# Optimization experiments

Measured on AMD Instinct MI355X. Metric: run time of the kernel, lower is better.

Reference implementation:

```python
import jax, jax.numpy as jnp
import numpy as np

N = 100000   # nodes
E = 1250000  # edges
G = 64       # graphs in batch
F_IN, H, NT, GT = 29, 64, 6, 4
L = 4        # num GCN layers


def setup_inputs() -> dict:
    key = jax.random.key(0)
    ks = jax.random.split(key, 14)
    s_in = 1.0 / np.sqrt(F_IN)
    s_h = 1.0 / np.sqrt(H)
    return {
        "x": jax.random.normal(ks[0], (N, F_IN), dtype=jnp.float32),
        "edge_index": jax.random.randint(ks[1], (2, E), 0, N, dtype=jnp.int64),
        "batch": jnp.sort(jax.random.randint(ks[2], (N,), 0, G, dtype=jnp.int64)),
        "encW": jax.random.uniform(ks[3], (F_IN, H), jnp.float32, -s_in, s_in),
        "encb": jax.random.uniform(ks[4], (H,), jnp.float32, -s_in, s_in),
        "convW": jax.random.uniform(ks[5], (L, H, H), jnp.float32, -s_h, s_h),
        "convb": jax.random.uniform(ks[6], (L, H), jnp.float32, -s_h, s_h),
        "nodeW": jax.random.uniform(ks[7], (H, NT), jnp.float32, -s_h, s_h),
        "nodeb": jax.random.uniform(ks[8], (NT,), jnp.float32, -s_h, s_h),
        "g1W": jax.random.uniform(ks[9], (H, H), jnp.float32, -s_h, s_h),
        "g1b": jax.random.uniform(ks[10], (H,), jnp.float32, -s_h, s_h),
        "g2W": jax.random.uniform(ks[11], (H, GT), jnp.float32, -s_h, s_h),
        "g2b": jax.random.uniform(ks[12], (GT,), jnp.float32, -s_h, s_h),
    }


def reference(x, edge_index, batch, encW, encb, convW, convb, nodeW, nodeb, g1W, g1b, g2W, g2b):
    # GCNConv with self-loops and symmetric normalization (PyG defaults)
    loop = jnp.arange(N, dtype=edge_index.dtype)
    row = jnp.concatenate([edge_index[0], loop])  # senders
    col = jnp.concatenate([edge_index[1], loop])  # receivers
    deg = jax.ops.segment_sum(jnp.ones_like(col, dtype=x.dtype), col, num_segments=N)
    dis = jnp.where(deg > 0, deg ** -0.5, 0.0)
    norm = (dis[row] * dis[col])[:, None]  # [E+N, 1]

    h = jax.nn.relu(x @ encW + encb)
    for i in range(L):
        hw = h @ convW[i]  # transform then propagate
        agg = jax.ops.segment_sum(hw[row] * norm, col, num_segments=N)
        h = jax.nn.relu(agg + convb[i])

    pred_node = h @ nodeW + nodeb

    counts = jax.ops.segment_sum(jnp.ones((N,), x.dtype), batch, num_segments=G)
    gemb = jax.ops.segment_sum(h, batch, num_segments=G) / jnp.maximum(counts, 1.0)[:, None]
    pred_global = jax.nn.relu(gemb @ g1W + g1b) @ g2W + g2b
    return (pred_node, pred_global)
```

## Files before the change

kernel.cpp:

```cpp
#include <hip/hip_runtime.h>
#include <hip/hip_fp16.h>

#define N_NODES 100000
#define N_EDGES 1250000
#define N_GRAPHS 64
#define F_INN 29
#define HD 64
#define NT 6
#define GT 4
#define NLAYERS 4
#define RECS_CAP 3000000
#define NBLK 1563
#define NBUK 782
#define HGRID 256
#define GB_BLOCKS 391
#define ENC_BLOCKS 6250
#define NH_BLOCKS 3125

typedef __attribute__((ext_vector_type(8))) _Float16 f16x8;
typedef __attribute__((ext_vector_type(4))) float f32x4;

__global__ void hist1_misc(const int* __restrict__ col, int* __restrict__ ghistT, int E,
                           const float* __restrict__ convW, uint4* __restrict__ wfrag,
                           __half* __restrict__ ht1, __half* __restrict__ ht2,
                           const int* __restrict__ batch, int* __restrict__ start) {
    __shared__ int lh[NBUK];
    int tid = threadIdx.x, b = blockIdx.x;
    if (b < HGRID) {
        for (int i = tid; i < NBUK; i += 256) lh[i] = 0;
        __syncthreads();
        for (int e = b * 256 + tid; e < E; e += HGRID * 256) atomicAdd(&lh[col[e] >> 7], 1);
        __syncthreads();
        for (int i = tid; i < NBUK; i += 256) ghistT[i * 256 + b] = lh[i];
    } else if (b < HGRID + 4) {
        int layer = b - HGRID;
        const float* W = convW + (size_t)layer * HD * HD;
        uint4* out = wfrag + (size_t)layer * 512;
        for (int s = tid; s < 512; s += 256) {
            int jt = s >> 7, ks = (s >> 6) & 1, l = s & 63;
            int j = jt * 16 + (l & 15);
            int k0 = ks * 32 + (l >> 4) * 8;
            __align__(16) __half hh[8];
            #pragma unroll
            for (int i = 0; i < 8; ++i) hh[i] = __float2half_rn(W[(size_t)(k0 + i) * HD + j]);
            out[s] = *reinterpret_cast<const uint4*>(hh);
        }
    } else if (b == HGRID + 4) {
        if (tid < HD) ht1[(size_t)N_NODES * HD + tid] = __float2half_rn(0.f);
        else if (tid < 2 * HD) ht2[(size_t)N_NODES * HD + (tid - HD)] = __float2half_rn(0.f);
    } else {
        int i = (b - HGRID - 5) * 256 + tid;
        if (i < N_NODES) {
            int bb = batch[i];
            if (i == 0) {
                for (int g = 0; g <= bb; ++g) start[g] = 0;
            } else {
                int pb = batch[i - 1];
                if (pb != bb) for (int g = pb + 1; g <= bb; ++g) start[g] = i;
            }
            if (i == N_NODES - 1) {
                for (int g = bb + 1; g <= N_GRAPHS; ++g) start[g] = N_NODES;
            }
        }
    }
}

__global__ void hist_colscan(int* __restrict__ ghistT, int* __restrict__ tot) {
    __shared__ int wsum[4];
    int k = blockIdx.x, tid = threadIdx.x;
    int v = ghistT[k * 256 + tid];
    int incl = v;
    int lane = tid & 63;
    #pragma unroll
    for (int off = 1; off < 64; off <<= 1) {
        int t = __shfl_up(incl, (unsigned)off, 64);
        if (lane >= off) incl += t;
    }
    if (lane == 63) wsum[tid >> 6] = incl;
    __syncthreads();
    int woff = 0;
    for (int w = 0; w < (tid >> 6); ++w) woff += wsum[w];
    ghistT[k * 256 + tid] = woff + incl - v;
    if (tid == 255) tot[k] = woff + incl;
}

__global__ void scan1(const int* __restrict__ in, int* __restrict__ out,
                      int* __restrict__ bsums, int n) {
    __shared__ int wsum[4];
    int tid = threadIdx.x;
    int base = blockIdx.x * 1024 + tid * 4;
    int v0 = (base + 0 < n) ? in[base + 0] : 0;
    int v1 = (base + 1 < n) ? in[base + 1] : 0;
    int v2 = (base + 2 < n) ? in[base + 2] : 0;
    int v3 = (base + 3 < n) ? in[base + 3] : 0;
    int tsum = v0 + v1 + v2 + v3;
    int incl = tsum;
    int lane = tid & 63;
    #pragma unroll
    for (int off = 1; off < 64; off <<= 1) {
        int t = __shfl_up(incl, (unsigned)off, 64);
        if (lane >= off) incl += t;
    }
    if (lane == 63) wsum[tid >> 6] = incl;
    __syncthreads();
    int woff = 0;
    for (int w = 0; w < (tid >> 6); ++w) woff += wsum[w];
    int run = woff + incl - tsum;
    if (base + 0 < n) out[base + 0] = run; run += v0;
    if (base + 1 < n) out[base + 1] = run; run += v1;
    if (base + 2 < n) out[base + 2] = run; run += v2;
    if (base + 3 < n) out[base + 3] = run;
    if (tid == 255) bsums[blockIdx.x] = woff + incl;
}

__global__ void scatter_buckets(const int* __restrict__ row, const int* __restrict__ col,
                                const int* __restrict__ ghistT, const int* __restrict__ boff,
                                unsigned* __restrict__ bke, int E) {
    __shared__ int cur[NBUK];
    int tid = threadIdx.x, b = blockIdx.x;
    for (int i = tid; i < NBUK; i += 256) cur[i] = ghistT[i * 256 + b] + boff[i];
    __syncthreads();
    for (int e = b * 256 + tid; e < E; e += HGRID * 256) {
        int c = col[e];
        int pos = atomicAdd(&cur[c >> 7], 1);
        bke[pos] = (unsigned)row[e] | ((unsigned)(c & 127) << 25);
    }
}

__global__ void bucket_count(const unsigned* __restrict__ bke, const int* __restrict__ boff,
                             int* __restrict__ cnt16, float* __restrict__ dis,
                             int* __restrict__ btot, int E) {
    __shared__ int lc[128];
    __shared__ int red[2];
    int k = blockIdx.x, tid = threadIdx.x;
    if (tid < 128) lc[tid] = 0;
    __syncthreads();
    int s = boff[k];
    int t = (k == NBUK - 1) ? E : boff[k + 1];
    for (int i = s + tid; i < t; i += 256) atomicAdd(&lc[bke[i] >> 25], 1);
    __syncthreads();
    int c16 = 0;
    if (tid < 128) {
        int node = k * 128 + tid;
        if (node < N_NODES) {
            int c = lc[tid];
            c16 = (c + 15) & ~15;
            cnt16[node] = c16;
            dis[node] = rsqrtf((float)(c + 1));
        }
        int sum = c16;
        #pragma unroll
        for (int off = 1; off < 64; off <<= 1) sum += __shfl_xor(sum, off, 64);
        if ((tid & 63) == 0) red[tid >> 6] = sum;
    }
    __syncthreads();
    if (tid == 0) btot[k] = red[0] + red[1];
}

__global__ void fill_enc(const unsigned* __restrict__ bke, const int* __restrict__ boff,
                         const int* __restrict__ bbase, const int* __restrict__ cnt16,
                         int* __restrict__ offs, int* __restrict__ srcs, int E,
                         const float* __restrict__ x, const float* __restrict__ encW,
                         const float* __restrict__ encb, const float* __restrict__ dis,
                         __half* __restrict__ ht) {
    int tid = threadIdx.x;
    int b = blockIdx.x;
    if (b < NBUK) {
        __shared__ int offsL[128];
        __shared__ int cur[128];
        __shared__ int wtot[2];
        int k = b;
        int v = 0, incl = 0;
        if (tid < 128) {
            int node = k * 128 + tid;
            v = (node < N_NODES) ? cnt16[node] : 0;
            incl = v;
            int lane = tid & 63;
            #pragma unroll
            for (int off = 1; off < 64; off <<= 1) {
                int t = __shfl_up(incl, (unsigned)off, 64);
                if (lane >= off) incl += t;
            }
            if (lane == 63) wtot[tid >> 6] = incl;
        }
        __syncthreads();
        if (tid < 128) {
            int w0 = (tid >= 64) ? wtot[0] : 0;
            int node = k * 128 + tid;
            int o = bbase[k] + w0 + incl - v;
            offsL[tid] = o;
            cur[tid] = 0;
            if (node < N_NODES) offs[node] = o;
        }
        __syncthreads();
        int s = boff[k];
        int t = (k == NBUK - 1) ? E : boff[k + 1];
        for (int i = s + tid; i < t; i += 256) {
            unsigned u = bke[i];
            int l = u >> 25;
            int r = atomicAdd(&cur[l], 1);
            srcs[offsL[l] + r] = (int)(u & 0x01FFFFFFu);
        }
        __syncthreads();
        if (tid < 128) {
            int node = k * 128 + tid;
            if (node < N_NODES) {
                int c = cur[tid];
                int c16 = (c + 15) & ~15;
                int base = offsL[tid];
                for (int p = base + c; p < base + c16; ++p) srcs[p] = N_NODES;
            }
        }
    } else {
        __shared__ float Ws[F_INN * HD];
        __shared__ float bs[HD];
        __shared__ float xs[16 * F_INN];
        for (int i = tid; i < F_INN * HD; i += 256) Ws[i] = encW[i];
        if (tid < HD) bs[tid] = encb[tid];
        int n0 = (b - NBUK) * 16;
        for (int i = tid; i < 16 * F_INN; i += 256) {
            int nn = n0 + i / F_INN;
            xs[i] = (nn < N_NODES) ? x[(size_t)nn * F_INN + (i % F_INN)] : 0.f;
        }
        __syncthreads();
        #pragma unroll
        for (int it = 0; it < 4; ++it) {
            int l = it * 4 + (tid >> 6);
            int j = tid & 63;
            int nn = n0 + l;
            if (nn < N_NODES) {
                float a = bs[j];
                #pragma unroll
                for (int k = 0; k < F_INN; ++k) a = fmaf(xs[l * F_INN + k], Ws[k * HD + j], a);
                ht[(size_t)nn * HD + j] = __float2half_rn(dis[nn] * fmaxf(a, 0.f));
            }
        }
    }
}


__device__ __forceinline__ float4 cvtrow(uint2 u) {
    float2 a = __half22float2(*reinterpret_cast<const __half2*>(&u.x));
    float2 b = __half22float2(*reinterpret_cast<const __half2*>(&u.y));
    return make_float4(a.x, a.y, b.x, b.y);
}

#define ROW16(src) (*reinterpret_cast<const uint2*>(&ht[(size_t)(src) * HD + fh]))
#define H2(u) (*reinterpret_cast<const __half2*>(&(u)))
#define ACC4T(r0, r1, r2, r3) { \
    __half2 ax = __hadd2(__hadd2(H2(r0.x), H2(r1.x)), __hadd2(H2(r2.x), H2(r3.x))); \
    __half2 ay = __hadd2(__hadd2(H2(r0.y), H2(r1.y)), __hadd2(H2(r2.y), H2(r3.y))); \
    float2 fx = __half22float2(ax); \
    float2 fy = __half22float2(ay); \
    acc.x += fx.x; acc.y += fx.y; acc.z += fy.x; acc.w += fy.y; }

__global__ void layer_kernel(const __half* __restrict__ ht,
                             const int* __restrict__ offs, const int* __restrict__ cnt16,
                             const int4* __restrict__ srcs4,
                             const float* __restrict__ dis,
                             const uint4* __restrict__ wfragL, const float* __restrict__ bias,
                             __half* __restrict__ hout, int scaleOut) {
    __shared__ uint4 WfS[512];
    __shared__ __half aggS[64 * 72];
    __shared__ int offsS[64];
    __shared__ int cntS[64];
    __shared__ float disS[64];
    int tid = threadIdx.x;
    int b = blockIdx.x;
    WfS[tid] = wfragL[tid];
    WfS[tid + 256] = wfragL[tid + 256];
    if (tid < 64) {
        int d = b * 64 + tid;
        if (d < N_NODES) {
            offsS[tid] = offs[d];
            cntS[tid] = cnt16[d];
            disS[tid] = dis[d];
        } else {
            offsS[tid] = offs[N_NODES - 1] + cnt16[N_NODES - 1];
            cntS[tid] = 0;
            disS[tid] = 0.f;
        }
    }
    __syncthreads();

    int wave = tid >> 6;
    int lane = tid & 63;
    int q = lane >> 4;
    int fh = (lane & 15) * 4;

    int l0 = wave * 16 + q * 4;
    {
        int nbase = b * 64 + l0;
        *reinterpret_cast<uint2*>(&aggS[(l0 + 0) * 72 + fh]) = ROW16(min(nbase + 0, N_NODES));
        *reinterpret_cast<uint2*>(&aggS[(l0 + 1) * 72 + fh]) = ROW16(min(nbase + 1, N_NODES));
        *reinterpret_cast<uint2*>(&aggS[(l0 + 2) * 72 + fh]) = ROW16(min(nbase + 2, N_NODES));
        *reinterpret_cast<uint2*>(&aggS[(l0 + 3) * 72 + fh]) = ROW16(min(nbase + 3, N_NODES));
    }
    int s = offsS[l0];
    int e = offsS[l0 + 3] + cntS[l0 + 3];
    int dcur = l0;
    int nb = offsS[l0] + cntS[l0];
    float4 acc = {0.f, 0.f, 0.f, 0.f};

    auto flush = [&](int d) {
        uint2 sv = *reinterpret_cast<uint2*>(&aggS[d * 72 + fh]);
        float4 sf = cvtrow(sv);
        acc.x += sf.x; acc.y += sf.y; acc.z += sf.z; acc.w += sf.w;
        __half2 h0 = __floats2half2_rn(acc.x, acc.y);
        __half2 h1 = __floats2half2_rn(acc.z, acc.w);
        uint2 w;
        w.x = *(unsigned*)&h0;
        w.y = *(unsigned*)&h1;
        *reinterpret_cast<uint2*>(&aggS[d * 72 + fh]) = w;
        acc = make_float4(0.f, 0.f, 0.f, 0.f);
    };

    for (int p = s; p < e; p += 16) {
        while (p >= nb) {
            flush(dcur);
            ++dcur;
            nb = offsS[dcur] + cntS[dcur];
        }
        int base = p >> 2;
        int4 e0 = srcs4[base + 0];
        int4 e1 = srcs4[base + 1];
        int4 e2 = srcs4[base + 2];
        int4 e3 = srcs4[base + 3];
        uint2 r0 = ROW16(e0.x), r1 = ROW16(e0.y), r2 = ROW16(e0.z), r3 = ROW16(e0.w);
        uint2 r4 = ROW16(e1.x), r5 = ROW16(e1.y), r6 = ROW16(e1.z), r7 = ROW16(e1.w);
        uint2 r8 = ROW16(e2.x), r9 = ROW16(e2.y), r10 = ROW16(e2.z), r11 = ROW16(e2.w);
        uint2 r12 = ROW16(e3.x), r13 = ROW16(e3.y), r14 = ROW16(e3.z), r15 = ROW16(e3.w);
        ACC4T(r0, r1, r2, r3);
        ACC4T(r4, r5, r6, r7);
        ACC4T(r8, r9, r10, r11);
        ACC4T(r12, r13, r14, r15);
    }
    while (dcur <= l0 + 3) {
        flush(dcur);
        ++dcur;
    }
    __syncthreads();

    f32x4 c0 = {0.f, 0.f, 0.f, 0.f}, c1 = c0, c2 = c0, c3 = c0;
    #pragma unroll
    for (int ks = 0; ks < 2; ++ks) {
        f16x8 bf = *reinterpret_cast<const f16x8*>(&WfS[(wave * 2 + ks) * 64 + lane]);
        f16x8 a0 = *reinterpret_cast<const f16x8*>(&aggS[(0 * 16 + (lane & 15)) * 72 + ks * 32 + (lane >> 4) * 8]);
        c0 = __builtin_amdgcn_mfma_f32_16x16x32_f16(a0, bf, c0, 0, 0, 0);
        f16x8 a1 = *reinterpret_cast<const f16x8*>(&aggS[(1 * 16 + (lane & 15)) * 72 + ks * 32 + (lane >> 4) * 8]);
        c1 = __builtin_amdgcn_mfma_f32_16x16x32_f16(a1, bf, c1, 0, 0, 0);
        f16x8 a2 = *reinterpret_cast<const f16x8*>(&aggS[(2 * 16 + (lane & 15)) * 72 + ks * 32 + (lane >> 4) * 8]);
        c2 = __builtin_amdgcn_mfma_f32_16x16x32_f16(a2, bf, c2, 0, 0, 0);
        f16x8 a3 = *reinterpret_cast<const f16x8*>(&aggS[(3 * 16 + (lane & 15)) * 72 + ks * 32 + (lane >> 4) * 8]);
        c3 = __builtin_amdgcn_mfma_f32_16x16x32_f16(a3, bf, c3, 0, 0, 0);
    }
    int j = wave * 16 + (lane & 15);
    float bj = bias[j];
    #pragma unroll
    for (int nt = 0; nt < 4; ++nt) {
        f32x4 c = (nt == 0) ? c0 : (nt == 1) ? c1 : (nt == 2) ? c2 : c3;
        #pragma unroll
        for (int i = 0; i < 4; ++i) {
            int rl = nt * 16 + (lane >> 4) * 4 + i;
            int node = b * 64 + rl;
            if (node < N_NODES) {
                float dn = disS[rl];
                float o = fmaxf(fmaf(dn, c[i], bj), 0.f);
                if (scaleOut) o *= dn;
                hout[(size_t)node * HD + j] = __float2half_rn(o);
            }
        }
    }
}

__global__ void heads_kernel(const __half* __restrict__ h, const float* __restrict__ W,
                             const float* __restrict__ bb, float* __restrict__ out,
                             const int* __restrict__ start, float* __restrict__ gpart) {
    int tid = threadIdx.x;
    int b = blockIdx.x;
    if (b < NH_BLOCKS) {
        __shared__ float Ws[HD * NT];
        __shared__ float bs[NT];
        __shared__ float hs[32 * 65];
        for (int i = tid; i < HD * NT; i += 256) Ws[i] = W[i];
        if (tid < NT) bs[tid] = bb[tid];
        int n0 = b * 32;
        const unsigned* hrow = reinterpret_cast<const unsigned*>(&h[(size_t)n0 * HD]);
        for (int i = tid; i < 32 * HD / 2; i += 256) {
            unsigned u = hrow[i];
            float2 f = __half22float2(*reinterpret_cast<const __half2*>(&u));
            int el = i * 2;
            int row = el >> 6, colc = el & 63;
            hs[row * 65 + colc] = f.x;
            hs[row * 65 + colc + 1] = f.y;
        }
        __syncthreads();
        int l = tid >> 3, t = tid & 7;
        int nn = n0 + l;
        if (nn < N_NODES && t < NT) {
            float a = bs[t];
            #pragma unroll
            for (int k = 0; k < HD; ++k) a = fmaf(hs[l * 65 + k], Ws[k * NT + t], a);
            out[(size_t)nn * NT + t] = a;
        }
    } else {
        __shared__ float red[4][HD];
        int pb = b - NH_BLOCKS;
        int g = pb >> 2, q = pb & 3;
        int s0 = start[g], e0 = start[g + 1];
        int len = e0 - s0;
        int qs = s0 + (len * q) / 4;
        int qe = s0 + (len * (q + 1)) / 4;
        int wave = tid >> 6, lane = tid & 63;
        float acc = 0.f;
        for (int r = qs + wave; r < qe; r += 4) acc += __half2float(h[(size_t)r * HD + lane]);
        red[wave][lane] = acc;
        __syncthreads();
        if (wave == 0)
            gpart[(size_t)pb * HD + lane] =
                red[0][lane] + red[1][lane] + red[2][lane] + red[3][lane];
    }
}

__global__ void global_head(const float* __restrict__ gpart, const int* __restrict__ start,
                            const float* __restrict__ g1W, const float* __restrict__ g1b,
                            const float* __restrict__ g2W, const float* __restrict__ g2b,
                            float* __restrict__ out) {
    __shared__ float rS[HD];
    int g = blockIdx.x;
    int j = threadIdx.x;
    int cnt = start[g + 1] - start[g];
    float inv = 1.f / fmaxf((float)cnt, 1.f);
    rS[j] = (gpart[(size_t)(4 * g + 0) * HD + j] + gpart[(size_t)(4 * g + 1) * HD + j] +
             gpart[(size_t)(4 * g + 2) * HD + j] + gpart[(size_t)(4 * g + 3) * HD + j]) * inv;
    __syncthreads();
    float a = g1b[j];
    #pragma unroll
    for (int k = 0; k < HD; ++k) a = fmaf(rS[k], g1W[k * HD + j], a);
    a = fmaxf(a, 0.f);
    float o0 = a * g2W[j * GT + 0];
    float o1 = a * g2W[j * GT + 1];
    float o2 = a * g2W[j * GT + 2];
    float o3 = a * g2W[j * GT + 3];
    #pragma unroll
    for (int off = 1; off < 64; off <<= 1) {
        o0 += __shfl_xor(o0, off, 64);
        o1 += __shfl_xor(o1, off, 64);
        o2 += __shfl_xor(o2, off, 64);
        o3 += __shfl_xor(o3, off, 64);
    }
    if (j == 0) {
        out[g * GT + 0] = o0 + g2b[0];
        out[g * GT + 1] = o1 + g2b[1];
        out[g * GT + 2] = o2 + g2b[2];
        out[g * GT + 3] = o3 + g2b[3];
    }
}


extern "C" void kernel_launch(void* const* d_in, const int* in_sizes, int n_in,
                              void* d_out, int out_size, void* d_ws, size_t ws_size,
                              hipStream_t stream) {
    const float* x    = (const float*)d_in[0];
    const int*   ei   = (const int*)d_in[1];
    const int*   batch= (const int*)d_in[2];
    const float* encW = (const float*)d_in[3];
    const float* encb = (const float*)d_in[4];
    const float* convW= (const float*)d_in[5];
    const float* convb= (const float*)d_in[6];
    const float* nodeW= (const float*)d_in[7];
    const float* nodeb= (const float*)d_in[8];
    const float* g1W  = (const float*)d_in[9];
    const float* g1b  = (const float*)d_in[10];
    const float* g2W  = (const float*)d_in[11];
    const float* g2b  = (const float*)d_in[12];
    float* out = (float*)d_out;

    const int N = N_NODES, E = N_EDGES;

    char* ws = (char*)d_ws;
    size_t off = 0;
    auto alloc = [&](size_t bytes) -> void* {
        void* p = ws + off;
        off += (bytes + 255) & ~(size_t)255;
        return p;
    };
    int*    ghistT = (int*)alloc((size_t)NBUK * 256 * 4);
    int*    tot    = (int*)alloc((size_t)NBUK * 4);
    int*    boff   = (int*)alloc((size_t)NBUK * 4);
    int*    btot   = (int*)alloc((size_t)NBUK * 4);
    int*    bbase  = (int*)alloc((size_t)NBUK * 4);
    unsigned* bke  = (unsigned*)alloc((size_t)E * 4);
    int*    offs   = (int*)alloc((size_t)N * 4);
    int*    cnt16  = (int*)alloc((size_t)N * 4);
    float*  dis    = (float*)alloc((size_t)N * 4);
    int*    bsums  = (int*)alloc(256 * 4);
    int*    start  = (int*)alloc((size_t)(N_GRAPHS + 1) * 4);
    float*  gpart  = (float*)alloc((size_t)N_GRAPHS * 4 * HD * 4);
    uint4*  wfrag  = (uint4*)alloc((size_t)NLAYERS * 512 * 16);
    int*    srcs   = (int*)alloc((size_t)RECS_CAP * 4);
    __half* ht1    = (__half*)alloc((size_t)(N + 1) * HD * 2);
    __half* ht2    = (__half*)alloc((size_t)(N + 1) * HD * 2);

    hist1_misc<<<HGRID + 5 + GB_BLOCKS, 256, 0, stream>>>(ei + E, ghistT, E, convW, wfrag,
                                                          ht1, ht2, batch, start);
    hist_colscan<<<NBUK, 256, 0, stream>>>(ghistT, tot);
    scan1<<<1, 256, 0, stream>>>(tot, boff, bsums, NBUK);
    scatter_buckets<<<HGRID, 256, 0, stream>>>(ei, ei + E, ghistT, boff, bke, E);
    bucket_count<<<NBUK, 256, 0, stream>>>(bke, boff, cnt16, dis, btot, E);
    scan1<<<1, 256, 0, stream>>>(btot, bbase, bsums, NBUK);
    fill_enc<<<NBUK + ENC_BLOCKS, 256, 0, stream>>>(bke, boff, bbase, cnt16, offs, srcs, E,
                                                    x, encW, encb, dis, ht1);

    __half* hin = ht1;
    __half* hot = ht2;
    for (int i = 0; i < NLAYERS; ++i) {
        layer_kernel<<<NBLK, 256, 0, stream>>>(hin, offs, cnt16, (const int4*)srcs, dis,
                                               wfrag + (size_t)i * 512,
                                               convb + (size_t)i * HD,
                                               hot, (i < NLAYERS - 1) ? 1 : 0);
        __half* t = hin; hin = hot; hot = t;
    }

    heads_kernel<<<NH_BLOCKS + N_GRAPHS * 4, 256, 0, stream>>>(hin, nodeW, nodeb, out,
                                                               start, gpart);
    global_head<<<N_GRAPHS, 64, 0, stream>>>(gpart, start, g1W, g1b, g2W, g2b, out + (size_t)N * NT);
}
```

Baseline: 233.4 us.

## Partition each node's edge list by source chunk for cache locality in gather

Edges of each destination node are split into four segments by source-node range, with each segment padded to a multiple of 4 instead of 16. The layer kernel then gathers one source chunk at a time across all nodes in a block, so the set of feature rows touched at once fits better in cache. Padding waste drops, but the gather loop now issues fewer loads per iteration, there are more segment boundaries, and the block keeps fp32 partial sums in shared memory. Weight fragments are read from global memory instead of being staged in shared memory, and launch bounds are added to raise occupancy.

After: 248.3 us. +6.4%, slower.

```diff
diff --git a/kernel.cpp b/kernel.cpp
--- a/kernel.cpp
+++ b/kernel.cpp
@@ -2,6 +2,7 @@
 #include <hip/hip_fp16.h>
 
 #define N_NODES 100000
+#define N_CAP 100096
 #define N_EDGES 1250000
 #define N_GRAPHS 64
 #define F_INN 29
@@ -9,6 +10,8 @@
 #define NT 6
 #define GT 4
 #define NLAYERS 4
+#define NC 4
+#define CHUNK_SZ 25000
 #define RECS_CAP 3000000
 #define NBLK 1563
 #define NBUK 782
@@ -128,69 +131,89 @@
 }
 
 __global__ void bucket_count(const unsigned* __restrict__ bke, const int* __restrict__ boff,
-                             int* __restrict__ cnt16, float* __restrict__ dis,
+                             int* __restrict__ cnt4c, float* __restrict__ dis,
                              int* __restrict__ btot, int E) {
-    __shared__ int lc[128];
-    __shared__ int red[2];
+    __shared__ int lc[128 * NC];
+    __shared__ int red[4];
     int k = blockIdx.x, tid = threadIdx.x;
-    if (tid < 128) lc[tid] = 0;
+    for (int i = tid; i < 128 * NC; i += 256) lc[i] = 0;
     __syncthreads();
     int s = boff[k];
     int t = (k == NBUK - 1) ? E : boff[k + 1];
-    for (int i = s + tid; i < t; i += 256) atomicAdd(&lc[bke[i] >> 25], 1);
-    __syncthreads();
-    int c16 = 0;
+    for (int i = s + tid; i < t; i += 256) {
+        unsigned u = bke[i];
+        int l = u >> 25;
+        unsigned src = u & 0x01FFFFFFu;
+        atomicAdd(&lc[l * NC + (int)(src / CHUNK_SZ)], 1);
+    }
+    __syncthreads();
+    int padsum = 0;
+    for (int i = tid; i < 128 * NC; i += 256) {
+        int p4 = (lc[i] + 3) & ~3;
+        int node = k * 128 + (i >> 2);
+        cnt4c[(size_t)node * NC + (i & 3)] = p4;
+        padsum += p4;
+    }
     if (tid < 128) {
         int node = k * 128 + tid;
         if (node < N_NODES) {
-            int c = lc[tid];
-            c16 = (c + 15) & ~15;
-            cnt16[node] = c16;
-            dis[node] = rsqrtf((float)(c + 1));
-        }
-        int sum = c16;
-        #pragma unroll
-        for (int off = 1; off < 64; off <<= 1) sum += __shfl_xor(sum, off, 64);
-        if ((tid & 63) == 0) red[tid >> 6] = sum;
-    }
-    __syncthreads();
-    if (tid == 0) btot[k] = red[0] + red[1];
+            int deg = lc[tid * NC] + lc[tid * NC + 1] + lc[tid * NC + 2] + lc[tid * NC + 3];
+            dis[node] = rsqrtf((float)(deg + 1));
+        }
+    }
+    int lane = tid & 63;
+    #pragma unroll
+    for (int off = 1; off < 64; off <<= 1) padsum += __shfl_xor(padsum, off, 64);
+    if (lane == 0) red[tid >> 6] = padsum;
+    __syncthreads();
+    if (tid == 0) btot[k] = red[0] + red[1] + red[2] + red[3];
 }
 
 __global__ void fill_enc(const unsigned* __restrict__ bke, const int* __restrict__ boff,
-                         const int* __restrict__ bbase, const int* __restrict__ cnt16,
-                         int* __restrict__ offs, int* __restrict__ srcs, int E,
+                         const int* __restrict__ bbase, const int* __restrict__ cnt4c,
+                         int* __restrict__ segoff, int* __restrict__ srcs, int E,
                          const float* __restrict__ x, const float* __restrict__ encW,
                          const float* __restrict__ encb, const float* __restrict__ dis,
                          __half* __restrict__ ht) {
+    __shared__ int segL[512];
+    __shared__ int curO[512];
+    __shared__ int wsum[4];
+    __shared__ float Ws[F_INN * HD];
+    __shared__ float bs[HD];
+    __shared__ float xs[16 * F_INN];
     int tid = threadIdx.x;
     int b = blockIdx.x;
     if (b < NBUK) {
-        __shared__ int offsL[128];
-        __shared__ int cur[128];
-        __shared__ int wtot[2];
         int k = b;
-        int v = 0, incl = 0;
-        if (tid < 128) {
-            int node = k * 128 + tid;
-            v = (node < N_NODES) ? cnt16[node] : 0;
-            incl = v;
-            int lane = tid & 63;
-            #pragma unroll
-            for (int off = 1; off < 64; off <<= 1) {
-                int t = __shfl_up(incl, (unsigned)off, 64);
-                if (lane >= off) incl += t;
-            }
-            if (lane == 63) wtot[tid >> 6] = incl;
-        }
-        __syncthreads();
-        if (tid < 128) {
-            int w0 = (tid >= 64) ? wtot[0] : 0;
-            int node = k * 128 + tid;
-            int o = bbase[k] + w0 + incl - v;
-            offsL[tid] = o;
-            cur[tid] = 0;
-            if (node < N_NODES) offs[node] = o;
+        int e0 = tid * 2, e1 = tid * 2 + 1;
+        auto padof = [&](int e) -> int {
+            int l = ((e >> 8) << 6) | (e & 63);
+            int c = (e >> 6) & 3;
+            return cnt4c[(size_t)(k * 128 + l) * NC + c];
+        };
+        int v0 = padof(e0), v1 = padof(e1);
+        int tsum = v0 + v1;
+        int incl = tsum;
+        int lane = tid & 63;
+        #pragma unroll
+        for (int off = 1; off < 64; off <<= 1) {
+            int t = __shfl_up(incl, (unsigned)off, 64);
+            if (lane >= off) incl += t;
+        }
+        if (lane == 63) wsum[tid >> 6] = incl;
+        __syncthreads();
+        int woff = 0;
+        for (int w = 0; w < (tid >> 6); ++w) woff += wsum[w];
+        int base = bbase[k] + woff + incl - tsum;
+        segL[e0] = base;
+        segL[e1] = base + v0;
+        curO[e0] = 0;
+        curO[e1] = 0;
+        {
+            int l0 = ((e0 >> 8) << 6) | (e0 & 63), c0 = (e0 >> 6) & 3;
+            int l1 = ((e1 >> 8) << 6) | (e1 & 63), c1 = (e1 >> 6) & 3;
+            segoff[(size_t)(k * 128 + l0) * NC + c0] = base;
+            segoff[(size_t)(k * 128 + l1) * NC + c1] = base + v0;
         }
         __syncthreads();
         int s = boff[k];
@@ -198,23 +221,20 @@
         for (int i = s + tid; i < t; i += 256) {
             unsigned u = bke[i];
             int l = u >> 25;
-            int r = atomicAdd(&cur[l], 1);
-            srcs[offsL[l] + r] = (int)(u & 0x01FFFFFFu);
-        }
-        __syncthreads();
-        if (tid < 128) {
-            int node = k * 128 + tid;
-            if (node < N_NODES) {
-                int c = cur[tid];
-                int c16 = (c + 15) & ~15;
-                int base = offsL[tid];
-                for (int p = base + c; p < base + c16; ++p) srcs[p] = N_NODES;
-            }
+            unsigned src = u & 0x01FFFFFFu;
+            int c = (int)(src / CHUNK_SZ);
+            int oi = ((l >> 6) << 8) | (c << 6) | (l & 63);
+            int r = atomicAdd(&curO[oi], 1);
+            srcs[segL[oi] + r] = (int)src;
+        }
+        __syncthreads();
+        {
+            int raw0 = curO[e0], st0 = segL[e0];
+            for (int p = st0 + raw0; p < st0 + v0; ++p) srcs[p] = N_NODES;
+            int raw1 = curO[e1], st1 = segL[e1];
+            for (int p = st1 + raw1; p < st1 + v1; ++p) srcs[p] = N_NODES;
         }
     } else {
-        __shared__ float Ws[F_INN * HD];
-        __shared__ float bs[HD];
-        __shared__ float xs[16 * F_INN];
         for (int i = tid; i < F_INN * HD; i += 256) Ws[i] = encW[i];
         if (tid < HD) bs[tid] = encb[tid];
         int n0 = (b - NBUK) * 16;
@@ -254,32 +274,24 @@
     float2 fy = __half22float2(ay); \
     acc.x += fx.x; acc.y += fx.y; acc.z += fy.x; acc.w += fy.y; }
 
-__global__ void layer_kernel(const __half* __restrict__ ht,
-                             const int* __restrict__ offs, const int* __restrict__ cnt16,
-                             const int4* __restrict__ srcs4,
-                             const float* __restrict__ dis,
-                             const uint4* __restrict__ wfragL, const float* __restrict__ bias,
-                             __half* __restrict__ hout, int scaleOut) {
-    __shared__ uint4 WfS[512];
-    __shared__ __half aggS[64 * 72];
-    __shared__ int offsS[64];
-    __shared__ int cntS[64];
+__global__ __launch_bounds__(256, 8)
+void layer_kernel(const __half* __restrict__ ht,
+                  const int* __restrict__ segoff, const int* __restrict__ cnt4c,
+                  const int4* __restrict__ srcs4,
+                  const float* __restrict__ dis,
+                  const uint4* __restrict__ wfragL, const float* __restrict__ bias,
+                  __half* __restrict__ hout, int scaleOut) {
+    __shared__ float aggS[64 * 68];
+    __shared__ int segS[256];
+    __shared__ int cntS[256];
     __shared__ float disS[64];
     int tid = threadIdx.x;
     int b = blockIdx.x;
-    WfS[tid] = wfragL[tid];
-    WfS[tid + 256] = wfragL[tid + 256];
+    segS[tid] = segoff[(size_t)b * 256 + tid];
+    cntS[tid] = cnt4c[(size_t)b * 256 + tid];
     if (tid < 64) {
         int d = b * 64 + tid;
-        if (d < N_NODES) {
-            offsS[tid] = offs[d];
-            cntS[tid] = cnt16[d];
-            disS[tid] = dis[d];
-        } else {
-            offsS[tid] = offs[N_NODES - 1] + cnt16[N_NODES - 1];
-            cntS[tid] = 0;
-            disS[tid] = 0.f;
-        }
+        disS[tid] = (d < N_NODES) ? dis[d] : 0.f;
     }
     __syncthreads();
 
@@ -291,68 +303,62 @@
     int l0 = wave * 16 + q * 4;
     {
         int nbase = b * 64 + l0;
-        *reinterpret_cast<uint2*>(&aggS[(l0 + 0) * 72 + fh]) = ROW16(min(nbase + 0, N_NODES));
-        *reinterpret_cast<uint2*>(&aggS[(l0 + 1) * 72 + fh]) = ROW16(min(nbase + 1, N_NODES));
-        *reinterpret_cast<uint2*>(&aggS[(l0 + 2) * 72 + fh]) = ROW16(min(nbase + 2, N_NODES));
-        *reinterpret_cast<uint2*>(&aggS[(l0 + 3) * 72 + fh]) = ROW16(min(nbase + 3, N_NODES));
-    }
-    int s = offsS[l0];
-    int e = offsS[l0 + 3] + cntS[l0 + 3];
-    int dcur = l0;
-    int nb = offsS[l0] + cntS[l0];
-    float4 acc = {0.f, 0.f, 0.f, 0.f};
-
-    auto flush = [&](int d) {
-        uint2 sv = *reinterpret_cast<uint2*>(&aggS[d * 72 + fh]);
-        float4 sf = cvtrow(sv);
-        acc.x += sf.x; acc.y += sf.y; acc.z += sf.z; acc.w += sf.w;
-        __half2 h0 = __floats2half2_rn(acc.x, acc.y);
-        __half2 h1 = __floats2half2_rn(acc.z, acc.w);
-        uint2 w;
-        w.x = *(unsigned*)&h0;
-        w.y = *(unsigned*)&h1;
-        *reinterpret_cast<uint2*>(&aggS[d * 72 + fh]) = w;
-        acc = make_float4(0.f, 0.f, 0.f, 0.f);
-    };
-
-    for (int p = s; p < e; p += 16) {
-        while (p >= nb) {
-            flush(dcur);
+        #pragma unroll
+        for (int d = 0; d < 4; ++d) {
+            float4 sf = cvtrow(ROW16(min(nbase + d, N_NODES)));
+            *reinterpret_cast<float4*>(&aggS[(l0 + d) * 68 + fh]) = sf;
+        }
+    }
+    #pragma unroll 1
+    for (int c = 0; c < NC; ++c) {
+        int dcur = l0;
+        int p = segS[l0 * 4 + c];
+        int pe = segS[(l0 + 3) * 4 + c] + cntS[(l0 + 3) * 4 + c];
+        int nb = p + cntS[l0 * 4 + c];
+        float4 acc = {0.f, 0.f, 0.f, 0.f};
+        for (; p < pe; p += 4) {
+            while (p >= nb) {
+                float4 cvv = *reinterpret_cast<float4*>(&aggS[dcur * 68 + fh]);
+                cvv.x += acc.x; cvv.y += acc.y; cvv.z += acc.z; cvv.w += acc.w;
+                *reinterpret_cast<float4*>(&aggS[dcur * 68 + fh]) = cvv;
+                acc = make_float4(0.f, 0.f, 0.f, 0.f);
+                ++dcur;
+                nb = segS[dcur * 4 + c] + cntS[dcur * 4 + c];
+            }
+            int4 e0 = srcs4[p >> 2];
+            uint2 r0 = ROW16(e0.x), r1 = ROW16(e0.y), r2 = ROW16(e0.z), r3 = ROW16(e0.w);
+            ACC4T(r0, r1, r2, r3);
+        }
+        while (dcur <= l0 + 3) {
+            float4 cvv = *reinterpret_cast<float4*>(&aggS[dcur * 68 + fh]);
+            cvv.x += acc.x; cvv.y += acc.y; cvv.z += acc.z; cvv.w += acc.w;
+            *reinterpret_cast<float4*>(&aggS[dcur * 68 + fh]) = cvv;
+            acc = make_float4(0.f, 0.f, 0.f, 0.f);
             ++dcur;
-            nb = offsS[dcur] + cntS[dcur];
-        }
-        int base = p >> 2;
-        int4 e0 = srcs4[base + 0];
-        int4 e1 = srcs4[base + 1];
-        int4 e2 = srcs4[base + 2];
-        int4 e3 = srcs4[base + 3];
-        uint2 r0 = ROW16(e0.x), r1 = ROW16(e0.y), r2 = ROW16(e0.z), r3 = ROW16(e0.w);
-        uint2 r4 = ROW16(e1.x), r5 = ROW16(e1.y), r6 = ROW16(e1.z), r7 = ROW16(e1.w);
-        uint2 r8 = ROW16(e2.x), r9 = ROW16(e2.y), r10 = ROW16(e2.z), r11 = ROW16(e2.w);
-        uint2 r12 = ROW16(e3.x), r13 = ROW16(e3.y), r14 = ROW16(e3.z), r15 = ROW16(e3.w);
-        ACC4T(r0, r1, r2, r3);
-        ACC4T(r4, r5, r6, r7);
-        ACC4T(r8, r9, r10, r11);
-        ACC4T(r12, r13, r14, r15);
-    }
-    while (dcur <= l0 + 3) {
-        flush(dcur);
-        ++dcur;
-    }
-    __syncthreads();
-
+        }
+    }
+    __syncthreads();
+
+    union AU { f16x8 v; __half2 h[4]; };
     f32x4 c0 = {0.f, 0.f, 0.f, 0.f}, c1 = c0, c2 = c0, c3 = c0;
     #pragma unroll
     for (int ks = 0; ks < 2; ++ks) {
-        f16x8 bf = *reinterpret_cast<const f16x8*>(&WfS[(wave * 2 + ks) * 64 + lane]);
-        f16x8 a0 = *reinterpret_cast<const f16x8*>(&aggS[(0 * 16 + (lane & 15)) * 72 + ks * 32 + (lane >> 4) * 8]);
-        c0 = __builtin_amdgcn_mfma_f32_16x16x32_f16(a0, bf, c0, 0, 0, 0);
-        f16x8 a1 = *reinterpret_cast<const f16x8*>(&aggS[(1 * 16 + (lane & 15)) * 72 + ks * 32 + (lane >> 4) * 8]);
-        c1 = __builtin_amdgcn_mfma_f32_16x16x32_f16(a1, bf, c1, 0, 0, 0);
-        f16x8 a2 = *reinterpret_cast<const f16x8*>(&aggS[(2 * 16 + (lane & 15)) * 72 + ks * 32 + (lane >> 4) * 8]);
-        c2 = __builtin_amdgcn_mfma_f32_16x16x32_f16(a2, bf, c2, 0, 0, 0);
-        f16x8 a3 = *reinterpret_cast<const f16x8*>(&aggS[(3 * 16 + (lane & 15)) * 72 + ks * 32 + (lane >> 4) * 8]);
-        c3 = __builtin_amdgcn_mfma_f32_16x16x32_f16(a3, bf, c3, 0, 0, 0);
+        f16x8 bf = *reinterpret_cast<const f16x8*>(&wfragL[(wave * 2 + ks) * 64 + lane]);
+        #pragma unroll
+        for (int nt = 0; nt < 4; ++nt) {
+            const float* ap = &aggS[(nt * 16 + (lane & 15)) * 68 + ks * 32 + (lane >> 4) * 8];
+            float4 f0 = *reinterpret_cast<const float4*>(ap);
+            float4 f1 = *reinterpret_cast<const float4*>(ap + 4);
+            AU u;
+            u.h[0] = __floats2half2_rn(f0.x, f0.y);
+            u.h[1] = __floats2half2_rn(f0.z, f0.w);
+            u.h[2] = __floats2half2_rn(f1.x, f1.y);
+            u.h[3] = __floats2half2_rn(f1.z, f1.w);
+            if (nt == 0) c0 = __builtin_amdgcn_mfma_f32_16x16x32_f16(u.v, bf, c0, 0, 0, 0);
+            else if (nt == 1) c1 = __builtin_amdgcn_mfma_f32_16x16x32_f16(u.v, bf, c1, 0, 0, 0);
+            else if (nt == 2) c2 = __builtin_amdgcn_mfma_f32_16x16x32_f16(u.v, bf, c2, 0, 0, 0);
+            else c3 = __builtin_amdgcn_mfma_f32_16x16x32_f16(u.v, bf, c3, 0, 0, 0);
+        }
     }
     int j = wave * 16 + (lane & 15);
     float bj = bias[j];
@@ -491,8 +497,8 @@
     int*    btot   = (int*)alloc((size_t)NBUK * 4);
     int*    bbase  = (int*)alloc((size_t)NBUK * 4);
     unsigned* bke  = (unsigned*)alloc((size_t)E * 4);
-    int*    offs   = (int*)alloc((size_t)N * 4);
-    int*    cnt16  = (int*)alloc((size_t)N * 4);
+    int*    cnt4c  = (int*)alloc((size_t)N_CAP * NC * 4);
+    int*    segoff = (int*)alloc((size_t)N_CAP * NC * 4);
     float*  dis    = (float*)alloc((size_t)N * 4);
     int*    bsums  = (int*)alloc(256 * 4);
     int*    start  = (int*)alloc((size_t)(N_GRAPHS + 1) * 4);
@@ -507,15 +513,15 @@
     hist_colscan<<<NBUK, 256, 0, stream>>>(ghistT, tot);
     scan1<<<1, 256, 0, stream>>>(tot, boff, bsums, NBUK);
     scatter_buckets<<<HGRID, 256, 0, stream>>>(ei, ei + E, ghistT, boff, bke, E);
-    bucket_count<<<NBUK, 256, 0, stream>>>(bke, boff, cnt16, dis, btot, E);
+    bucket_count<<<NBUK, 256, 0, stream>>>(bke, boff, cnt4c, dis, btot, E);
     scan1<<<1, 256, 0, stream>>>(btot, bbase, bsums, NBUK);
-    fill_enc<<<NBUK + ENC_BLOCKS, 256, 0, stream>>>(bke, boff, bbase, cnt16, offs, srcs, E,
+    fill_enc<<<NBUK + ENC_BLOCKS, 256, 0, stream>>>(bke, boff, bbase, cnt4c, segoff, srcs, E,
                                                     x, encW, encb, dis, ht1);
 
     __half* hin = ht1;
     __half* hot = ht2;
     for (int i = 0; i < NLAYERS; ++i) {
-        layer_kernel<<<NBLK, 256, 0, stream>>>(hin, offs, cnt16, (const int4*)srcs, dis,
+        layer_kernel<<<NBLK, 256, 0, stream>>>(hin, segoff, cnt4c, (const int4*)srcs, dis,
                                                wfrag + (size_t)i * 512,
                                                convb + (size_t)i * HD,
                                                hot, (i < NLAYERS - 1) ? 1 : 0);
```

## Prefetch edge indices and make each wave own its rows to drop block barrier

Applied to the files above, without the earlier changes.

The gather loop now loads the next batch of 16 source indices before the current rows are accumulated, a software prefetch meant to hide index-load latency. The MFMA stage is reorganised so each wave multiplies only the 16 aggregated rows it produced itself against all four weight column tiles. Because a wave no longer reads other waves' rows, the __syncthreads between aggregation and transform is removed. Bias is also staged in shared memory. The risk is correctness: the aggS rows written in flush are the wave's own rows, but the lanes that write them differ from the lanes that read them, and removing the barrier relies on wave-level LDS ordering.

Measured after the change: 225.7 us. 3.3% less time.

```diff
diff --git a/kernel.cpp b/kernel.cpp
--- a/kernel.cpp
+++ b/kernel.cpp
@@ -265,12 +265,14 @@
     __shared__ int offsS[64];
     __shared__ int cntS[64];
     __shared__ float disS[64];
+    __shared__ float biasS[64];
     int tid = threadIdx.x;
     int b = blockIdx.x;
     WfS[tid] = wfragL[tid];
     WfS[tid + 256] = wfragL[tid + 256];
     if (tid < 64) {
         int d = b * 64 + tid;
+        biasS[tid] = bias[tid];
         if (d < N_NODES) {
             offsS[tid] = offs[d];
             cntS[tid] = cnt16[d];
@@ -315,21 +317,32 @@
         acc = make_float4(0.f, 0.f, 0.f, 0.f);
     };
 
+    int4 i0, i1, i2, i3;
+    if (s < e) {
+        int base = s >> 2;
+        i0 = srcs4[base + 0];
+        i1 = srcs4[base + 1];
+        i2 = srcs4[base + 2];
+        i3 = srcs4[base + 3];
+    }
     for (int p = s; p < e; p += 16) {
+        uint2 r0 = ROW16(i0.x), r1 = ROW16(i0.y), r2 = ROW16(i0.z), r3 = ROW16(i0.w);
+        uint2 r4 = ROW16(i1.x), r5 = ROW16(i1.y), r6 = ROW16(i1.z), r7 = ROW16(i1.w);
+        uint2 r8 = ROW16(i2.x), r9 = ROW16(i2.y), r10 = ROW16(i2.z), r11 = ROW16(i2.w);
+        uint2 r12 = ROW16(i3.x), r13 = ROW16(i3.y), r14 = ROW16(i3.z), r15 = ROW16(i3.w);
+        int pn = p + 16;
+        if (pn < e) {
+            int base = pn >> 2;
+            i0 = srcs4[base + 0];
+            i1 = srcs4[base + 1];
+            i2 = srcs4[base + 2];
+            i3 = srcs4[base + 3];
+        }
         while (p >= nb) {
             flush(dcur);
             ++dcur;
             nb = offsS[dcur] + cntS[dcur];
         }
-        int base = p >> 2;
-        int4 e0 = srcs4[base + 0];
-        int4 e1 = srcs4[base + 1];
-        int4 e2 = srcs4[base + 2];
-        int4 e3 = srcs4[base + 3];
-        uint2 r0 = ROW16(e0.x), r1 = ROW16(e0.y), r2 = ROW16(e0.z), r3 = ROW16(e0.w);
-        uint2 r4 = ROW16(e1.x), r5 = ROW16(e1.y), r6 = ROW16(e1.z), r7 = ROW16(e1.w);
-        uint2 r8 = ROW16(e2.x), r9 = ROW16(e2.y), r10 = ROW16(e2.z), r11 = ROW16(e2.w);
-        uint2 r12 = ROW16(e3.x), r13 = ROW16(e3.y), r14 = ROW16(e3.z), r15 = ROW16(e3.w);
         ACC4T(r0, r1, r2, r3);
         ACC4T(r4, r5, r6, r7);
         ACC4T(r8, r9, r10, r11);
@@ -339,29 +352,29 @@
         flush(dcur);
         ++dcur;
     }
-    __syncthreads();
 
     f32x4 c0 = {0.f, 0.f, 0.f, 0.f}, c1 = c0, c2 = c0, c3 = c0;
     #pragma unroll
     for (int ks = 0; ks < 2; ++ks) {
-        f16x8 bf = *reinterpret_cast<const f16x8*>(&WfS[(wave * 2 + ks) * 64 + lane]);
-        f16x8 a0 = *reinterpret_cast<const f16x8*>(&aggS[(0 * 16 + (lane & 15)) * 72 + ks * 32 + (lane >> 4) * 8]);
-        c0 = __builtin_amdgcn_mfma_f32_16x16x32_f16(a0, bf, c0, 0, 0, 0);
-        f16x8 a1 = *reinterpret_cast<const f16x8*>(&aggS[(1 * 16 + (lane & 15)) * 72 + ks * 32 + (lane >> 4) * 8]);
-        c1 = __builtin_amdgcn_mfma_f32_16x16x32_f16(a1, bf, c1, 0, 0, 0);
-        f16x8 a2 = *reinterpret_cast<const f16x8*>(&aggS[(2 * 16 + (lane & 15)) * 72 + ks * 32 + (lane >> 4) * 8]);
-        c2 = __builtin_amdgcn_mfma_f32_16x16x32_f16(a2, bf, c2, 0, 0, 0);
-        f16x8 a3 = *reinterpret_cast<const f16x8*>(&aggS[(3 * 16 + (lane & 15)) * 72 + ks * 32 + (lane >> 4) * 8]);
-        c3 = __builtin_amdgcn_mfma_f32_16x16x32_f16(a3, bf, c3, 0, 0, 0);
-    }
-    int j = wave * 16 + (lane & 15);
-    float bj = bias[j];
+        f16x8 a = *reinterpret_cast<const f16x8*>(
+            &aggS[(wave * 16 + (lane & 15)) * 72 + ks * 32 + (lane >> 4) * 8]);
+        f16x8 b0 = *reinterpret_cast<const f16x8*>(&WfS[(0 * 2 + ks) * 64 + lane]);
+        c0 = __builtin_amdgcn_mfma_f32_16x16x32_f16(a, b0, c0, 0, 0, 0);
+        f16x8 b1 = *reinterpret_cast<const f16x8*>(&WfS[(1 * 2 + ks) * 64 + lane]);
+        c1 = __builtin_amdgcn_mfma_f32_16x16x32_f16(a, b1, c1, 0, 0, 0);
+        f16x8 b2 = *reinterpret_cast<const f16x8*>(&WfS[(2 * 2 + ks) * 64 + lane]);
+        c2 = __builtin_amdgcn_mfma_f32_16x16x32_f16(a, b2, c2, 0, 0, 0);
+        f16x8 b3 = *reinterpret_cast<const f16x8*>(&WfS[(3 * 2 + ks) * 64 + lane]);
+        c3 = __builtin_amdgcn_mfma_f32_16x16x32_f16(a, b3, c3, 0, 0, 0);
+    }
     #pragma unroll
-    for (int nt = 0; nt < 4; ++nt) {
-        f32x4 c = (nt == 0) ? c0 : (nt == 1) ? c1 : (nt == 2) ? c2 : c3;
+    for (int jt = 0; jt < 4; ++jt) {
+        f32x4 c = (jt == 0) ? c0 : (jt == 1) ? c1 : (jt == 2) ? c2 : c3;
+        int j = jt * 16 + (lane & 15);
+        float bj = biasS[j];
         #pragma unroll
         for (int i = 0; i < 4; ++i) {
-            int rl = nt * 16 + (lane >> 4) * 4 + i;
+            int rl = wave * 16 + (lane >> 4) * 4 + i;
             int node = b * 64 + rl;
             if (node < N_NODES) {
                 float dn = disS[rl];
```
